# Performance work log

Measured on AMD Instinct MI355X. Metric: run time of the kernel, lower is better.

Reference implementation:

```python
import jax, jax.numpy as jnp
import numpy as np

B, T, IN, H, OUT = 32, 2048, 256, 512, 256
DT = 0.1


def _orthogonal(key, n):
    a = jax.random.normal(key, (n, n), dtype=jnp.float32)
    q, r = jnp.linalg.qr(a)
    return q * jnp.sign(jnp.diag(r))[None, :]


def _xavier(key, fan_out, fan_in):
    bound = np.sqrt(6.0 / (fan_in + fan_out)).astype(np.float32)
    return jax.random.uniform(key, (fan_out, fan_in), minval=-bound, maxval=bound, dtype=jnp.float32)


def setup_inputs() -> dict:
    key = jax.random.key(0)
    ks = jax.random.split(key, 9)
    x = jax.random.normal(ks[0], (B, T, IN), dtype=jnp.float32)
    W_in0 = _xavier(ks[1], H, IN)
    b_in0 = jnp.zeros((H,), dtype=jnp.float32)
    W_rec0 = _orthogonal(ks[2], H)
    tau0 = jnp.clip(jax.random.uniform(ks[3], (H,), minval=0.5, maxval=2.0, dtype=jnp.float32), 0.1, 10.0)
    W_in1 = _xavier(ks[4], H, H)
    b_in1 = jnp.zeros((H,), dtype=jnp.float32)
    W_rec1 = _orthogonal(ks[5], H)
    tau1 = jnp.clip(jax.random.uniform(ks[6], (H,), minval=0.5, maxval=2.0, dtype=jnp.float32), 0.1, 10.0)
    bound = np.sqrt(1.0 / H).astype(np.float32)
    W_out = jax.random.uniform(ks[7], (OUT, H), minval=-bound, maxval=bound, dtype=jnp.float32)
    b_out = jax.random.uniform(ks[8], (OUT,), minval=-bound, maxval=bound, dtype=jnp.float32)
    return {"x": x, "W_in0": W_in0, "b_in0": b_in0, "W_rec0": W_rec0, "tau0": tau0,
            "W_in1": W_in1, "b_in1": b_in1, "W_rec1": W_rec1, "tau1": tau1,
            "W_out": W_out, "b_out": b_out}


def _cell(x_t, h, W_in, b_in, W_rec, tau):
    # CT-RNN Euler step: h + dt * (act(W_in x + W_rec h) - h) / clamp(tau)
    tau_c = jnp.clip(tau, 0.1, 10.0)
    target = jnp.tanh(x_t @ W_in.T + b_in + h @ W_rec.T)
    return h + DT * (target - h) / tau_c


def reference(x, W_in0, b_in0, W_rec0, tau0, W_in1, b_in1, W_rec1, tau1, W_out, b_out):
    def step(carry, x_t):
        h0, h1 = carry
        h0 = _cell(x_t, h0, W_in0, b_in0, W_rec0, tau0)
        h1 = _cell(h0, h1, W_in1, b_in1, W_rec1, tau1)
        out_t = h1 @ W_out.T + b_out  # [B, OUT]
        return (h0, h1), out_t

    h0 = jnp.zeros((x.shape[0], H), dtype=x.dtype)
    h1 = jnp.zeros((x.shape[0], H), dtype=x.dtype)
    xs = jnp.swapaxes(x, 0, 1)  # [T, B, IN]
    _, outs = jax.lax.scan(step, (h0, h1), xs)
    out = jnp.swapaxes(outs, 0, 1)  # [B, T, OUT]
    return out + x  # use_residual since input_size == output_size
```

## Files before the change

kernel.cpp:

```cpp
#include <hip/hip_runtime.h>
#include <cstdint>
#include <cstddef>

typedef __attribute__((ext_vector_type(8))) short short8;
typedef __attribute__((ext_vector_type(4))) short short4v;
typedef __attribute__((ext_vector_type(4))) float f32x4;

#define TT 2048
#define BB 32
#define HH 512

__device__ inline short f2bf(float f) {
  union { float f; unsigned u; } v; v.f = f;
  unsigned r = v.u + 0x7fffu + ((v.u >> 16) & 1u);
  return (short)(r >> 16);
}
__device__ inline float bf2f(short s) {
  union { unsigned u; float f; } v; v.u = ((unsigned)(unsigned short)s) << 16;
  return v.f;
}


__global__ void convert_weights(const float* __restrict__ w0, const float* __restrict__ w1,
                                const float* __restrict__ w2, const float* __restrict__ w3,
                                const float* __restrict__ w4, short* __restrict__ dst) {
  int i = blockIdx.x * 256 + threadIdx.x;
  if (i >= 1048576) return;
  const float* src; int off;
  if (i < 131072)      { src = w0; off = i; }
  else if (i < 393216) { src = w1; off = i - 131072; }
  else if (i < 655360) { src = w2; off = i - 393216; }
  else if (i < 917504) { src = w3; off = i - 655360; }
  else                 { src = w4; off = i - 917504; }
  dst[i] = f2bf(src[off]);
}

template<int A_XF32, int OUT_SW, int RESID>
__global__ __launch_bounds__(256) void gemm_bt(const void* __restrict__ Ap,
    const short* __restrict__ Bw, const float* __restrict__ bias,
    const float* __restrict__ resid, void* __restrict__ Cp, int M, int N, int K) {
  __shared__ short As[64][40];
  __shared__ short Bs[64][40];
  int tid = threadIdx.x;
  int m0 = blockIdx.x * 64, n0 = blockIdx.y * 64;
  int w = tid >> 6, lane = tid & 63;
  int wm = w >> 1, wn = w & 1;
  int quad = lane >> 4, l16 = lane & 15;
  f32x4 acc[2][2];
#pragma unroll
  for (int i = 0; i < 2; i++)
#pragma unroll
    for (int j = 0; j < 2; j++) acc[i][j] = (f32x4){0.f, 0.f, 0.f, 0.f};
  int lr = tid >> 2, lk = (tid & 3) * 8;
  for (int kk = 0; kk < K; kk += 32) {
    __syncthreads();
    {
      int rl = m0 + lr;
      if (A_XF32) {
        const float* A = (const float*)Ap;
        size_t phys = ((size_t)(rl & 31) * TT + (rl >> 5)) * K;
        const float4* p = (const float4*)(A + phys + kk + lk);
        float4 a0 = p[0], a1 = p[1];
        short8 v;
        v[0] = f2bf(a0.x); v[1] = f2bf(a0.y); v[2] = f2bf(a0.z); v[3] = f2bf(a0.w);
        v[4] = f2bf(a1.x); v[5] = f2bf(a1.y); v[6] = f2bf(a1.z); v[7] = f2bf(a1.w);
        *(short8*)&As[lr][lk] = v;
      } else {
        const short* A = (const short*)Ap;
        *(short8*)&As[lr][lk] = *(const short8*)(A + (size_t)rl * K + kk + lk);
      }
      *(short8*)&Bs[lr][lk] = *(const short8*)(Bw + (size_t)(n0 + lr) * K + kk + lk);
    }
    __syncthreads();
    short8 af[2], bfr[2];
#pragma unroll
    for (int i = 0; i < 2; i++) af[i] = *(short8*)&As[wm * 32 + i * 16 + l16][quad * 8];
#pragma unroll
    for (int j = 0; j < 2; j++) bfr[j] = *(short8*)&Bs[wn * 32 + j * 16 + l16][quad * 8];
#pragma unroll
    for (int i = 0; i < 2; i++)
#pragma unroll
      for (int j = 0; j < 2; j++)
        acc[i][j] = __builtin_amdgcn_mfma_f32_16x16x32_bf16(af[i], bfr[j], acc[i][j], 0, 0, 0);
  }
#pragma unroll
  for (int i = 0; i < 2; i++) {
#pragma unroll
    for (int j = 0; j < 2; j++) {
#pragma unroll
      for (int rr = 0; rr < 4; rr++) {
        int row = m0 + wm * 32 + i * 16 + quad * 4 + rr;
        int col = n0 + wn * 32 + j * 16 + l16;
        float v2 = acc[i][j][rr] + bias[col];
        if (OUT_SW) {
          int t = row >> 5, b = row & 31;
          int wg = b >> 4, bl = b & 15, q2 = bl >> 2, r2 = bl & 3;
          int wv2 = col >> 6, ct2 = (col >> 4) & 3, lc = col & 15;
          size_t idx = (((((size_t)t * 2 + wg) * 8 + wv2) * 4 + ct2) * 64 + (q2 * 16 + lc)) * 4 + r2;
          ((short*)Cp)[idx] = f2bf(v2);
        } else {
          size_t idx = ((size_t)(row & 31) * TT + (row >> 5)) * N + col;
          if (RESID) v2 += resid[idx];
          ((float*)Cp)[idx] = v2;
        }
      }
    }
  }
}

__global__ __launch_bounds__(512, 2) void seq_scan(
    const short* __restrict__ xin_sw, const short* __restrict__ Wrec,
    const float* __restrict__ tau, short* __restrict__ hall) {
  __shared__ short Wl[8][16][64][8];
  __shared__ short hb[16][520];
  int wg = blockIdx.x;
  int tid = threadIdx.x;
  int wv = tid >> 6, lane = tid & 63;
  int q = lane >> 4, l16 = lane & 15;
  int c0 = wv * 64;

  for (int i = tid; i < 16 * 520 / 2; i += 512) ((int*)hb)[i] = 0;

  short8 wreg[48];
#pragma unroll
  for (int ct = 0; ct < 4; ct++) {
    const short* wrow = Wrec + (size_t)(c0 + ct * 16 + l16) * HH;
#pragma unroll
    for (int kc = 0; kc < 12; kc++)
      wreg[ct * 12 + kc] = *(const short8*)(wrow + kc * 32 + q * 8);
#pragma unroll
    for (int kc = 12; kc < 16; kc++)
      *(short8*)&Wl[wv][ct * 4 + (kc - 12)][lane][0] = *(const short8*)(wrow + kc * 32 + q * 8);
  }
  float rate[4];
#pragma unroll
  for (int ct = 0; ct < 4; ct++) {
    float tc = tau[c0 + ct * 16 + l16];
    tc = fminf(fmaxf(tc, 0.1f), 10.f);
    rate[ct] = 0.1f / tc;
  }
  float st[16];
#pragma unroll
  for (int i = 0; i < 16; i++) st[i] = 0.f;

  short4v xr[4];
#pragma unroll
  for (int ct = 0; ct < 4; ct++)
    xr[ct] = *(const short4v*)(xin_sw + ((((size_t)0 * 2 + wg) * 8 + wv) * 4 + ct) * 256 + lane * 4);
  __syncthreads();

  for (int t = 0; t < TT; t++) {
    f32x4 acc[4];
#pragma unroll
    for (int ct = 0; ct < 4; ct++) acc[ct] = (f32x4){0.f, 0.f, 0.f, 0.f};
#pragma unroll
    for (int kc = 0; kc < 16; kc++) {
      short8 af = *(short8*)&hb[l16][kc * 32 + q * 8];
#pragma unroll
      for (int ct = 0; ct < 4; ct++) {
        short8 wf;
        if (kc < 12) wf = wreg[ct * 12 + kc];
        else wf = *(short8*)&Wl[wv][ct * 4 + (kc - 12)][lane][0];
        acc[ct] = __builtin_amdgcn_mfma_f32_16x16x32_bf16(af, wf, acc[ct], 0, 0, 0);
      }
    }
    __syncthreads();
#pragma unroll
    for (int ct = 0; ct < 4; ct++) {
#pragma unroll
      for (int r = 0; r < 4; r++) {
        float u = acc[ct][r] + bf2f(xr[ct][r]);
        float a = fabsf(u);
        float e = exp2f(a * 2.8853900817779268f);
        float tg = copysignf(1.f - 2.f / (e + 1.f), u);
        float h = st[ct * 4 + r];
        h += rate[ct] * (tg - h);
        st[ct * 4 + r] = h;
        hb[q * 4 + r][c0 + ct * 16 + l16] = f2bf(h);
      }
    }
    if (t + 1 < TT) {
#pragma unroll
      for (int ct = 0; ct < 4; ct++)
        xr[ct] = *(const short4v*)(xin_sw + ((((size_t)(t + 1) * 2 + wg) * 8 + wv) * 4 + ct) * 256 + lane * 4);
    }
    __syncthreads();
#pragma unroll
    for (int it = 0; it < 2; it++) {
      int ci = it * 512 + tid;
      int bl = ci >> 6, off = (ci & 63) * 8;
      short8 v = *(short8*)&hb[bl][off];
      *(short8*)(hall + ((size_t)t * 32 + wg * 16 + bl) * HH + off) = v;
    }
  }
}

extern "C" void kernel_launch(void* const* d_in, const int* in_sizes, int n_in,
                              void* d_out, int out_size, void* d_ws, size_t ws_size,
                              hipStream_t stream) {
  const float* x      = (const float*)d_in[0];
  const float* W_in0  = (const float*)d_in[1];
  const float* b_in0  = (const float*)d_in[2];
  const float* W_rec0 = (const float*)d_in[3];
  const float* tau0   = (const float*)d_in[4];
  const float* W_in1  = (const float*)d_in[5];
  const float* b_in1  = (const float*)d_in[6];
  const float* W_rec1 = (const float*)d_in[7];
  const float* tau1   = (const float*)d_in[8];
  const float* W_out  = (const float*)d_in[9];
  const float* b_out  = (const float*)d_in[10];

  char* ws = (char*)d_ws;
  short* wb     = (short*)ws;
  short* xin_sw = (short*)(ws + (4u << 20));
  short* hall   = (short*)(ws + (68u << 20));

  short* wbin0  = wb;
  short* wbrec0 = wb + 131072;
  short* wbin1  = wb + 393216;
  short* wbrec1 = wb + 655360;
  short* wbout  = wb + 917504;

  convert_weights<<<4096, 256, 0, stream>>>(W_in0, W_rec0, W_in1, W_rec1, W_out, wb);

  dim3 g1(1024, 8);
  gemm_bt<1, 1, 0><<<g1, 256, 0, stream>>>((const void*)x, wbin0, b_in0, nullptr,
                                           (void*)xin_sw, BB * TT, HH, 256);
  seq_scan<<<2, 512, 0, stream>>>(xin_sw, wbrec0, tau0, hall);
  gemm_bt<0, 1, 0><<<g1, 256, 0, stream>>>((const void*)hall, wbin1, b_in1, nullptr,
                                           (void*)xin_sw, BB * TT, HH, HH);
  seq_scan<<<2, 512, 0, stream>>>(xin_sw, wbrec1, tau1, hall);
  dim3 g2(1024, 4);
  gemm_bt<0, 0, 1><<<g2, 256, 0, stream>>>((const void*)hall, wbout, b_out, x,
                                           d_out, BB * TT, 256, HH);
}
```

Before: 14.78 ms.

## Double-buffer hidden state, keep all recurrent weights in registers, transpose MFMA operands

The sequential scan kernel now double-buffers the hidden-state LDS tile, which drops one of the two barriers per timestep. It holds the full recurrent weight slice in registers instead of spilling part of it to LDS, and swaps the MFMA operands so each lane's outputs are contiguous columns. That lets it write packed short4 values to LDS and global memory directly from registers, with the writeback deferred one step. The x-projection prefetch is issued earlier, tanh uses hardware exp2/rcp with clamping, and the GEMM's swizzled output layout is changed to match. The risk is register pressure (64 short8 weight registers) lowering occupancy or causing spills, plus slightly different tanh accuracy.

```diff
diff --git a/kernel.cpp b/kernel.cpp
--- a/kernel.cpp
+++ b/kernel.cpp
@@ -94,9 +94,9 @@
         float v2 = acc[i][j][rr] + bias[col];
         if (OUT_SW) {
           int t = row >> 5, b = row & 31;
-          int wg = b >> 4, bl = b & 15, q2 = bl >> 2, r2 = bl & 3;
-          int wv2 = col >> 6, ct2 = (col >> 4) & 3, lc = col & 15;
-          size_t idx = (((((size_t)t * 2 + wg) * 8 + wv2) * 4 + ct2) * 64 + (q2 * 16 + lc)) * 4 + r2;
+          int wg2 = b >> 4, bl = b & 15;
+          int wv2 = col >> 6, ct2 = (col >> 4) & 3, q2 = (col >> 2) & 3, r2 = col & 3;
+          size_t idx = (((((size_t)t * 2 + wg2) * 8 + wv2) * 4 + ct2) * 64 + (q2 * 16 + bl)) * 4 + r2;
           ((short*)Cp)[idx] = f2bf(v2);
         } else {
           size_t idx = ((size_t)(row & 31) * TT + (row >> 5)) * N + col;
@@ -111,87 +111,95 @@
 __global__ __launch_bounds__(512, 2) void seq_scan(
     const short* __restrict__ xin_sw, const short* __restrict__ Wrec,
     const float* __restrict__ tau, short* __restrict__ hall) {
-  __shared__ short Wl[8][16][64][8];
-  __shared__ short hb[16][520];
+  __shared__ __align__(16) short hb[2][16][520];
   int wg = blockIdx.x;
   int tid = threadIdx.x;
   int wv = tid >> 6, lane = tid & 63;
   int q = lane >> 4, l16 = lane & 15;
   int c0 = wv * 64;
 
-  for (int i = tid; i < 16 * 520 / 2; i += 512) ((int*)hb)[i] = 0;
-
-  short8 wreg[48];
+  for (int i = tid; i < 2 * 16 * 520 / 2; i += 512) ((int*)hb)[i] = 0;
+
+  short8 wreg[64];
 #pragma unroll
   for (int ct = 0; ct < 4; ct++) {
     const short* wrow = Wrec + (size_t)(c0 + ct * 16 + l16) * HH;
 #pragma unroll
-    for (int kc = 0; kc < 12; kc++)
-      wreg[ct * 12 + kc] = *(const short8*)(wrow + kc * 32 + q * 8);
-#pragma unroll
-    for (int kc = 12; kc < 16; kc++)
-      *(short8*)&Wl[wv][ct * 4 + (kc - 12)][lane][0] = *(const short8*)(wrow + kc * 32 + q * 8);
-  }
-  float rate[4];
-#pragma unroll
-  for (int ct = 0; ct < 4; ct++) {
-    float tc = tau[c0 + ct * 16 + l16];
-    tc = fminf(fmaxf(tc, 0.1f), 10.f);
-    rate[ct] = 0.1f / tc;
-  }
+    for (int kc = 0; kc < 16; kc++)
+      wreg[ct * 16 + kc] = *(const short8*)(wrow + kc * 32 + q * 8);
+  }
+  float rate[16];
+#pragma unroll
+  for (int ct = 0; ct < 4; ct++)
+#pragma unroll
+    for (int r = 0; r < 4; r++) {
+      float tc = tau[c0 + ct * 16 + q * 4 + r];
+      tc = fminf(fmaxf(tc, 0.1f), 10.f);
+      rate[ct * 4 + r] = 0.1f / tc;
+    }
   float st[16];
 #pragma unroll
   for (int i = 0; i < 16; i++) st[i] = 0.f;
+  short4v hpk[4];
+#pragma unroll
+  for (int ct = 0; ct < 4; ct++) hpk[ct] = (short4v){0, 0, 0, 0};
+
+  const short* xbase = xin_sw + (size_t)wg * 8192 + wv * 1024 + lane * 4;
+  short* hallp = hall + ((size_t)wg * 16 + l16) * HH + c0 + q * 4;
 
   short4v xr[4];
 #pragma unroll
-  for (int ct = 0; ct < 4; ct++)
-    xr[ct] = *(const short4v*)(xin_sw + ((((size_t)0 * 2 + wg) * 8 + wv) * 4 + ct) * 256 + lane * 4);
+  for (int ct = 0; ct < 4; ct++) xr[ct] = *(const short4v*)(xbase + ct * 256);
   __syncthreads();
 
+  int cur = 0;
   for (int t = 0; t < TT; t++) {
+    int tn = (t + 1 < TT) ? t + 1 : t;
+    const short* xp = xbase + (size_t)tn * 16384;
+    short4v xn[4];
+#pragma unroll
+    for (int ct = 0; ct < 4; ct++) xn[ct] = *(const short4v*)(xp + ct * 256);
+    if (t > 0) {
+      short* hp = hallp + ((size_t)(t - 1) * 32) * HH;
+#pragma unroll
+      for (int ct = 0; ct < 4; ct++) *(short4v*)(hp + ct * 16) = hpk[ct];
+    }
     f32x4 acc[4];
 #pragma unroll
     for (int ct = 0; ct < 4; ct++) acc[ct] = (f32x4){0.f, 0.f, 0.f, 0.f};
 #pragma unroll
     for (int kc = 0; kc < 16; kc++) {
-      short8 af = *(short8*)&hb[l16][kc * 32 + q * 8];
-#pragma unroll
-      for (int ct = 0; ct < 4; ct++) {
-        short8 wf;
-        if (kc < 12) wf = wreg[ct * 12 + kc];
-        else wf = *(short8*)&Wl[wv][ct * 4 + (kc - 12)][lane][0];
-        acc[ct] = __builtin_amdgcn_mfma_f32_16x16x32_bf16(af, wf, acc[ct], 0, 0, 0);
-      }
-    }
-    __syncthreads();
+      short8 af = *(short8*)&hb[cur][l16][kc * 32 + q * 8];
+#pragma unroll
+      for (int ct = 0; ct < 4; ct++)
+        acc[ct] = __builtin_amdgcn_mfma_f32_16x16x32_bf16(wreg[ct * 16 + kc], af, acc[ct], 0, 0, 0);
+    }
 #pragma unroll
     for (int ct = 0; ct < 4; ct++) {
+      short4v hv;
 #pragma unroll
       for (int r = 0; r < 4; r++) {
         float u = acc[ct][r] + bf2f(xr[ct][r]);
-        float a = fabsf(u);
-        float e = exp2f(a * 2.8853900817779268f);
-        float tg = copysignf(1.f - 2.f / (e + 1.f), u);
+        float v = u * 2.8853900817779268f;
+        v = fminf(fmaxf(v, -30.f), 30.f);
+        float e = __builtin_amdgcn_exp2f(v);
+        float tg = (e - 1.f) * __builtin_amdgcn_rcpf(e + 1.f);
         float h = st[ct * 4 + r];
-        h += rate[ct] * (tg - h);
+        h += rate[ct * 4 + r] * (tg - h);
         st[ct * 4 + r] = h;
-        hb[q * 4 + r][c0 + ct * 16 + l16] = f2bf(h);
+        hv[r] = f2bf(h);
       }
-    }
-    if (t + 1 < TT) {
-#pragma unroll
-      for (int ct = 0; ct < 4; ct++)
-        xr[ct] = *(const short4v*)(xin_sw + ((((size_t)(t + 1) * 2 + wg) * 8 + wv) * 4 + ct) * 256 + lane * 4);
+      hpk[ct] = hv;
+      *(short4v*)&hb[cur ^ 1][l16][c0 + ct * 16 + q * 4] = hv;
+      xr[ct] = xn[ct];
     }
     __syncthreads();
-#pragma unroll
-    for (int it = 0; it < 2; it++) {
-      int ci = it * 512 + tid;
-      int bl = ci >> 6, off = (ci & 63) * 8;
-      short8 v = *(short8*)&hb[bl][off];
-      *(short8*)(hall + ((size_t)t * 32 + wg * 16 + bl) * HH + off) = v;
-    }
+    cur ^= 1;
+  }
+  {
+    short* hp = hallp + ((size_t)(TT - 1) * 32) * HH;
+#pragma unroll
+    for (int ct = 0; ct < 4; ct++) *(short4v*)(hp + ct * 16) = hpk[ct];
   }
 }
 
```

Measured after the change: 29.02 ms. 96.4% more time.

## Transpose scan MFMA operands, vectorize h writes, lighter barriers and fast tanh

Applied to the files above, without the earlier changes.

The recurrent scan now swaps the MFMA operand order so each lane holds four consecutive hidden columns for one batch row. This lets h be written to LDS and global memory as packed short4 vectors, instead of through a separate copy-out phase after an extra barrier. The input-projection GEMM output layout and the per-lane tau rates change to match. Barriers become raw s_waitcnt plus s_barrier, tanh uses the hardware exp2 and rcp intrinsics with clamping, and the x prefetch is double-buffered by unrolling two steps. The risks are small accuracy differences from the approximate rcp, and the correctness of the hand-written barrier since global stores are not waited on.

```diff
diff --git a/kernel.cpp b/kernel.cpp
--- a/kernel.cpp
+++ b/kernel.cpp
@@ -18,6 +18,10 @@
 __device__ inline float bf2f(short s) {
   union { unsigned u; float f; } v; v.u = ((unsigned)(unsigned short)s) << 16;
   return v.f;
+}
+
+__device__ inline void barrier_lds() {
+  asm volatile("s_waitcnt lgkmcnt(0)\n\ts_barrier" ::: "memory");
 }
 
 
@@ -94,9 +98,9 @@
         float v2 = acc[i][j][rr] + bias[col];
         if (OUT_SW) {
           int t = row >> 5, b = row & 31;
-          int wg = b >> 4, bl = b & 15, q2 = bl >> 2, r2 = bl & 3;
-          int wv2 = col >> 6, ct2 = (col >> 4) & 3, lc = col & 15;
-          size_t idx = (((((size_t)t * 2 + wg) * 8 + wv2) * 4 + ct2) * 64 + (q2 * 16 + lc)) * 4 + r2;
+          int wg2 = b >> 4, bl = b & 15;
+          int wv2 = col >> 6, ct2 = (col >> 4) & 3, q2 = (col >> 2) & 3, r2 = col & 3;
+          size_t idx = (((((size_t)t * 2 + wg2) * 8 + wv2) * 4 + ct2) * 64 + (q2 * 16 + bl)) * 4 + r2;
           ((short*)Cp)[idx] = f2bf(v2);
         } else {
           size_t idx = ((size_t)(row & 31) * TT + (row >> 5)) * N + col;
@@ -112,7 +116,7 @@
     const short* __restrict__ xin_sw, const short* __restrict__ Wrec,
     const float* __restrict__ tau, short* __restrict__ hall) {
   __shared__ short Wl[8][16][64][8];
-  __shared__ short hb[16][520];
+  __shared__ __align__(16) short hb[16][520];
   int wg = blockIdx.x;
   int tid = threadIdx.x;
   int wv = tid >> 6, lane = tid & 63;
@@ -132,67 +136,81 @@
     for (int kc = 12; kc < 16; kc++)
       *(short8*)&Wl[wv][ct * 4 + (kc - 12)][lane][0] = *(const short8*)(wrow + kc * 32 + q * 8);
   }
-  float rate[4];
-#pragma unroll
-  for (int ct = 0; ct < 4; ct++) {
-    float tc = tau[c0 + ct * 16 + l16];
-    tc = fminf(fmaxf(tc, 0.1f), 10.f);
-    rate[ct] = 0.1f / tc;
-  }
+  float rate[16];
+#pragma unroll
+  for (int ct = 0; ct < 4; ct++)
+#pragma unroll
+    for (int r = 0; r < 4; r++) {
+      float tc = tau[c0 + ct * 16 + q * 4 + r];
+      tc = fminf(fmaxf(tc, 0.1f), 10.f);
+      rate[ct * 4 + r] = 0.1f / tc;
+    }
   float st[16];
 #pragma unroll
   for (int i = 0; i < 16; i++) st[i] = 0.f;
 
-  short4v xr[4];
-#pragma unroll
-  for (int ct = 0; ct < 4; ct++)
-    xr[ct] = *(const short4v*)(xin_sw + ((((size_t)0 * 2 + wg) * 8 + wv) * 4 + ct) * 256 + lane * 4);
+  const short* xbase = xin_sw + (size_t)wg * 8192 + wv * 1024 + lane * 4;
+  short* hallp = hall + ((size_t)wg * 16 + l16) * HH + c0 + q * 4;
+
+  short4v xrA[4], xrB[4];
+#pragma unroll
+  for (int ct = 0; ct < 4; ct++) xrA[ct] = *(const short4v*)(xbase + ct * 256);
   __syncthreads();
 
-  for (int t = 0; t < TT; t++) {
-    f32x4 acc[4];
-#pragma unroll
-    for (int ct = 0; ct < 4; ct++) acc[ct] = (f32x4){0.f, 0.f, 0.f, 0.f};
-#pragma unroll
-    for (int kc = 0; kc < 16; kc++) {
-      short8 af = *(short8*)&hb[l16][kc * 32 + q * 8];
-#pragma unroll
-      for (int ct = 0; ct < 4; ct++) {
-        short8 wf;
-        if (kc < 12) wf = wreg[ct * 12 + kc];
-        else wf = *(short8*)&Wl[wv][ct * 4 + (kc - 12)][lane][0];
-        acc[ct] = __builtin_amdgcn_mfma_f32_16x16x32_bf16(af, wf, acc[ct], 0, 0, 0);
-      }
-    }
-    __syncthreads();
-#pragma unroll
-    for (int ct = 0; ct < 4; ct++) {
-#pragma unroll
-      for (int r = 0; r < 4; r++) {
-        float u = acc[ct][r] + bf2f(xr[ct][r]);
-        float a = fabsf(u);
-        float e = exp2f(a * 2.8853900817779268f);
-        float tg = copysignf(1.f - 2.f / (e + 1.f), u);
-        float h = st[ct * 4 + r];
-        h += rate[ct] * (tg - h);
-        st[ct * 4 + r] = h;
-        hb[q * 4 + r][c0 + ct * 16 + l16] = f2bf(h);
-      }
-    }
-    if (t + 1 < TT) {
-#pragma unroll
-      for (int ct = 0; ct < 4; ct++)
-        xr[ct] = *(const short4v*)(xin_sw + ((((size_t)(t + 1) * 2 + wg) * 8 + wv) * 4 + ct) * 256 + lane * 4);
-    }
-    __syncthreads();
-#pragma unroll
-    for (int it = 0; it < 2; it++) {
-      int ci = it * 512 + tid;
-      int bl = ci >> 6, off = (ci & 63) * 8;
-      short8 v = *(short8*)&hb[bl][off];
-      *(short8*)(hall + ((size_t)t * 32 + wg * 16 + bl) * HH + off) = v;
-    }
-  }
+#define STEP_BODY(T, XU, XP)                                                      \
+  {                                                                               \
+    int tn = ((T) + 1 < TT) ? (T) + 1 : (T);                                      \
+    const short* xp_ = xbase + (size_t)tn * 16384;                                \
+    _Pragma("unroll")                                                             \
+    for (int ct = 0; ct < 4; ct++) XP[ct] = *(const short4v*)(xp_ + ct * 256);    \
+    f32x4 acc[4];                                                                 \
+    _Pragma("unroll")                                                             \
+    for (int ct = 0; ct < 4; ct++) acc[ct] = (f32x4){0.f, 0.f, 0.f, 0.f};         \
+    _Pragma("unroll")                                                             \
+    for (int kc = 0; kc < 12; kc++) {                                             \
+      short8 af = *(short8*)&hb[l16][kc * 32 + q * 8];                            \
+      _Pragma("unroll")                                                           \
+      for (int ct = 0; ct < 4; ct++)                                              \
+        acc[ct] = __builtin_amdgcn_mfma_f32_16x16x32_bf16(wreg[ct * 12 + kc],     \
+                                                          af, acc[ct], 0, 0, 0);  \
+    }                                                                             \
+    _Pragma("unroll")                                                             \
+    for (int kc = 12; kc < 16; kc++) {                                            \
+      short8 af = *(short8*)&hb[l16][kc * 32 + q * 8];                            \
+      _Pragma("unroll")                                                           \
+      for (int ct = 0; ct < 4; ct++) {                                            \
+        short8 wf = *(short8*)&Wl[wv][ct * 4 + (kc - 12)][lane][0];               \
+        acc[ct] = __builtin_amdgcn_mfma_f32_16x16x32_bf16(wf, af, acc[ct], 0, 0, 0); \
+      }                                                                           \
+    }                                                                             \
+    barrier_lds();                                 \
+    short* hp_ = hallp + ((size_t)(T) * 32) * HH;                                 \
+    _Pragma("unroll")                                                             \
+    for (int ct = 0; ct < 4; ct++) {                                              \
+      short4v hv;                                                                 \
+      _Pragma("unroll")                                                           \
+      for (int r = 0; r < 4; r++) {                                               \
+        float u = acc[ct][r] + bf2f(XU[ct][r]);                                   \
+        float v = u * 2.8853900817779268f;                                        \
+        v = fminf(fmaxf(v, -30.f), 30.f);                                         \
+        float e = __builtin_amdgcn_exp2f(v);                                      \
+        float tg = (e - 1.f) * __builtin_amdgcn_rcpf(e + 1.f);                    \
+        float h = st[ct * 4 + r];                                                 \
+        h += rate[ct * 4 + r] * (tg - h);                                         \
+        st[ct * 4 + r] = h;                                                       \
+        hv[r] = f2bf(h);                                                          \
+      }                                                                           \
+      *(short4v*)&hb[l16][c0 + ct * 16 + q * 4] = hv;                             \
+      *(short4v*)(hp_ + ct * 16) = hv;                                            \
+    }                                                                             \
+    barrier_lds();                                          \
+  }
+
+  for (int t = 0; t < TT; t += 2) {
+    STEP_BODY(t, xrA, xrB);
+    STEP_BODY(t + 1, xrB, xrA);
+  }
+#undef STEP_BODY
 }
 
 extern "C" void kernel_launch(void* const* d_in, const int* in_sizes, int n_in,
```

Measured after the change: 14.02 ms. 5.1% less time.
